# Kernel tuning notes

Hardware: AMD Instinct MI355X
Metric: run time of the kernel (lower is better)

## Reference

```python
import jax, jax.numpy as jnp
import numpy as np

IN_FEATURES = 1024
OUT_FEATURES = 1024
NUM_GRIDS = 8
GRID_MIN, GRID_MAX = -2.0, 2.0
DENOM = (GRID_MAX - GRID_MIN) / (NUM_GRIDS - 1)
LN_EPS = 1e-5
GRID = jnp.linspace(GRID_MIN, GRID_MAX, NUM_GRIDS)


def setup_inputs() -> dict:
    key = jax.random.key(0)
    k_x, k_sw, k_bw = jax.random.split(key, 3)
    N = 8192
    x = jax.random.normal(k_x, (N, IN_FEATURES), dtype=jnp.float32)
    ln_gamma = jnp.ones((IN_FEATURES,), dtype=jnp.float32)
    ln_beta = jnp.zeros((IN_FEATURES,), dtype=jnp.float32)
    # trunc_normal(std=0.1) approximated by scaled normal
    spline_w = 0.1 * jax.random.normal(k_sw, (OUT_FEATURES, IN_FEATURES * NUM_GRIDS), dtype=jnp.float32)
    base_w = jax.random.normal(k_bw, (OUT_FEATURES, IN_FEATURES), dtype=jnp.float32) * (1.0 / np.sqrt(IN_FEATURES))
    base_b = jnp.zeros((OUT_FEATURES,), dtype=jnp.float32)
    return {"x": x, "ln_gamma": ln_gamma, "ln_beta": ln_beta,
            "spline_w": spline_w, "base_w": base_w, "base_b": base_b}


def reference(x, ln_gamma, ln_beta, spline_w, base_w, base_b):
    # LayerNorm over last dim
    mu = jnp.mean(x, axis=-1, keepdims=True)
    var = jnp.var(x, axis=-1, keepdims=True)
    xn = (x - mu) * jax.lax.rsqrt(var + LN_EPS) * ln_gamma + ln_beta
    # RBF basis: [N, in, G]
    basis = jnp.exp(-jnp.square((xn[..., None] - GRID) / DENOM))
    basis = basis.reshape(x.shape[0], IN_FEATURES * NUM_GRIDS)
    y = jnp.einsum('nk,ok->no', basis, spline_w)
    y = y + jnp.einsum('nd,od->no', jax.nn.silu(x), base_w) + base_b
    return y
```

## Files before the change

kernel.cpp:

```cpp
#include <hip/hip_runtime.h>
#include <hip/hip_bf16.h>
#include <stdint.h>

#define IN_F 1024
#define OUT_F 1024
#define NG 8
#define KSPLINE 8192
#define KDIM 9216
#define KHALF 4608
#define M_ROWS 8192
#define LOG2E 1.4426950408889634f
#define KC 2.1019642153762872f

#define A_BLOCKS (M_ROWS / 4)
#define W_BLOCKS ((OUT_F * 2304) / 256)
#define RB (KDIM * 2)
#define GBOFF 131072

using half4v = __attribute__((ext_vector_type(4))) _Float16;
using half8  = __attribute__((ext_vector_type(8))) _Float16;
using f32x4  = __attribute__((ext_vector_type(4))) float;
using f32x2  = __attribute__((ext_vector_type(2))) float;

#define AS1 __attribute__((address_space(1)))
#define AS3 __attribute__((address_space(3)))

__global__ __launch_bounds__(256) void prep_kernel(
        const float* __restrict__ x, const float* __restrict__ sw,
        const float* __restrict__ bw, _Float16* __restrict__ S,
        float* __restrict__ musig, _Float16* __restrict__ W) {
    if (blockIdx.x >= A_BLOCKS) {
        int idx = (blockIdx.x - A_BLOCKS) * 256 + threadIdx.x;
        int o   = idx / 2304;
        int k4  = idx - o * 2304;
        f32x4 v;
        if (k4 < 2048) v = __builtin_nontemporal_load(&((const f32x4*)sw)[(size_t)o * 2048 + k4]);
        else           v = __builtin_nontemporal_load(&((const f32x4*)bw)[(size_t)o * 256 + (k4 - 2048)]);
        half4v h = { (_Float16)v.x, (_Float16)v.y, (_Float16)v.z, (_Float16)v.w };
        *(half4v*)(W + (size_t)idx * 4) = h;
        return;
    }
    const int wave = threadIdx.x >> 6, lane = threadIdx.x & 63;
    const int row = blockIdx.x * 4 + wave;
    const float* xr = x + (size_t)row * IN_F;

    float xv[16];
    float s = 0.0f, s2 = 0.0f;
#pragma unroll
    for (int j = 0; j < 16; ++j) {
        float v = xr[j * 64 + lane];
        xv[j] = v;
        s += v;
        s2 += v * v;
    }
#pragma unroll
    for (int off = 32; off > 0; off >>= 1) {
        s  += __shfl_xor(s, off);
        s2 += __shfl_xor(s2, off);
    }
    float mu   = s * (1.0f / IN_F);
    float var  = s2 * (1.0f / IN_F) - mu * mu;
    float rstd = rsqrtf(var + 1e-5f);
    if (lane == 0) {
        f32x2 ms; ms[0] = mu; ms[1] = rstd;
        ((f32x2*)musig)[row] = ms;
    }
    _Float16* Srow = S + (size_t)row * IN_F;
#pragma unroll
    for (int j = 0; j < 16; ++j) {
        float xs = xv[j];
        Srow[j * 64 + lane] = (_Float16)(xs / (1.0f + exp2f(-xs * LOG2E)));
    }
}

__device__ __forceinline__ half8 spline8(float xv, float mu, float rs, float gk, float bk) {
    const float cqg[8] = {
        -2.0000000f * KC, -1.4285715f * KC, -0.8571429f * KC, -0.2857143f * KC,
         0.2857143f * KC,  0.8571429f * KC,  1.4285715f * KC,  2.0000000f * KC };
    float xq = fmaf((xv - mu) * rs, gk, bk);
    half8 h;
#pragma unroll
    for (int g = 0; g < 8; ++g) {
        float d = xq - cqg[g];
        h[g] = (_Float16)__builtin_amdgcn_exp2f(-(d * d));
    }
    return h;
}

__global__ __launch_bounds__(512, 2) void gemm_kernel(
        const _Float16* __restrict__ W, const _Float16* __restrict__ S,
        const float* __restrict__ x, const float* __restrict__ musig,
        const float* __restrict__ gamma, const float* __restrict__ beta,
        const float* __restrict__ bias, float* __restrict__ C,
        float* __restrict__ P, int ntiles, int gpz) {
    extern __shared__ __align__(16) char smem[];
    const int tid  = threadIdx.x;
    const int wave = tid >> 6, lane = tid & 63;
    const int wm = wave >> 2, wn = wave & 3;

    const int lb = blockIdx.x;
    const int per_xcd = gridDim.x >> 5;
    const int xcd = lb & 7, sl = lb >> 3;
    const int g  = xcd * per_xcd + (sl >> 2);
    const int bn = sl & 3;
    const int bm = g / gpz;
    const int z  = g - bm * gpz;
    const int ksoff = z * KHALF;

    const int l8 = lane >> 3;
    const int chunkswz = ((lane & 7) ^ l8) << 4;
    const int gAr[4] = {0, 128, 64, 192};
    const int gB[4]  = {0, 128, 32, 160};
    const char* pB[4];
    const char* pS[4];
    const float* xp[4];
#pragma unroll
    for (int s = 0; s < 4; ++s) {
        pB[s] = (const char*)W + (size_t)(bn * 256 + gB[s] + (wave >> 2) * 64
                + (wave & 3) * 8 + l8) * RB + (size_t)ksoff * 2 + chunkswz;
        int arow = bm * 256 + gAr[s] + wave * 8 + l8;
        pS[s] = (const char*)S + (size_t)arow * (IN_F * 2) + chunkswz;
    }
    const int r6 = tid >> 3;
    const int c8 = tid & 7;
    const int wAbase = r6 * 128 + ((c8 ^ (r6 & 7)) << 4);
    float mu4[4], rs4[4];
#pragma unroll
    for (int s = 0; s < 4; ++s) {
        int arow = bm * 256 + gAr[s] + r6;
        xp[s] = x + (size_t)arow * IN_F;
        f32x2 ms = ((const f32x2*)musig)[arow];
        mu4[s] = ms[0]; rs4[s] = ms[1];
    }

#define STAGE_B(s, nb, colb) __builtin_amdgcn_global_load_lds( \
        (const AS1 void*)(pB[s] + (colb)), \
        (AS3 void*)(smem + (nb) + 32768 + (s) * 8192 + wave * 1024), 16, 0, 0)
#define STAGE_S(s, nb, colb) __builtin_amdgcn_global_load_lds( \
        (const AS1 void*)(pS[s] + (colb)), \
        (AS3 void*)(smem + (nb) + (s) * 8192 + wave * 1024), 16, 0, 0)

    const int lm  = lane & 15;
    const int hi  = (lane >> 4) << 4;
    const int swz = (lm & 7) << 4;
    const int ck0 = (0  + hi) ^ swz;
    const int ck1 = (64 + hi) ^ swz;
    const int aB0 = (0 + wm) * 8192 + lm * 128;
    const int aB1 = (2 + wm) * 8192 + lm * 128;
    const int bB0 = 32768 + (0 + (wn >> 1)) * 8192 + ((wn & 1) * 32 + lm) * 128;
    const int bB1 = 32768 + (2 + (wn >> 1)) * 8192 + ((wn & 1) * 32 + lm) * 128;

    f32x4 acc[8][4] = {};

#define MFMA_QUAD(MB, NB2, Aa, Bb)                                              \
    __builtin_amdgcn_s_barrier();                                               \
    asm volatile("s_waitcnt lgkmcnt(0)" ::: "memory");                          \
    __builtin_amdgcn_sched_barrier(0);                                          \
    __builtin_amdgcn_s_setprio(1);                                              \
    _Pragma("unroll")                                                           \
    for (int n = 0; n < 2; ++n)                                                 \
        _Pragma("unroll")                                                       \
        for (int m = 0; m < 4; ++m)                                             \
            acc[(MB)+m][(NB2)+n] = __builtin_amdgcn_mfma_f32_16x16x32_f16(      \
                Aa[m][0], Bb[n][0], acc[(MB)+m][(NB2)+n], 0, 0, 0);             \
    _Pragma("unroll")                                                           \
    for (int n = 0; n < 2; ++n)                                                 \
        _Pragma("unroll")                                                       \
        for (int m = 0; m < 4; ++m)                                             \
            acc[(MB)+m][(NB2)+n] = __builtin_amdgcn_mfma_f32_16x16x32_f16(      \
                Aa[m][1], Bb[n][1], acc[(MB)+m][(NB2)+n], 0, 0, 0);             \
    __builtin_amdgcn_s_setprio(0);                                              \
    __builtin_amdgcn_s_barrier();

    {
        f32x2 t0; t0[0] = gamma[tid] * KC;       t0[1] = beta[tid] * KC;
        f32x2 t1; t1[0] = gamma[tid + 512] * KC; t1[1] = beta[tid + 512] * KC;
        *(f32x2*)(smem + GBOFF + tid * 8) = t0;
        *(f32x2*)(smem + GBOFF + (tid + 512) * 8) = t1;
    }
    const int f00 = z * 576 + c8;
    float xf0[4];
#pragma unroll
    for (int s = 0; s < 4; ++s) xf0[s] = xp[s][f00];
    STAGE_B(0, 0, 0); STAGE_B(1, 0, 0); STAGE_B(2, 0, 0); STAGE_B(3, 0, 0);
    __syncthreads();
    {
        f32x2 gb0 = *(const f32x2*)(smem + GBOFF + f00 * 8);
#pragma unroll
        for (int s = 0; s < 4; ++s) {
            half8 h = spline8(xf0[s], mu4[s], rs4[s], gb0[0], gb0[1]);
            *(half8*)(smem + s * 8192 + wAbase) = h;
        }
    }
    asm volatile("s_waitcnt lgkmcnt(0)" ::: "memory");
    __builtin_amdgcn_s_barrier();

    for (int kt = 0; kt < ntiles; ++kt) {
        const int cb = (kt & 1) * 65536;
        const int nb = cb ^ 65536;
        const bool pref = (kt + 1 < ntiles);
        const int nk = ksoff + (kt + 1) * 64;
        const bool nsil = nk >= KSPLINE;
        const size_t bcolb = (size_t)(kt + 1) * 128;
        const int fb = z * 576 + (kt + 1) * 8 + c8;
        size_t scolb = 0;
        if (nsil) scolb = (size_t)(nk - KSPLINE) * 2;

        float xf[4];
        if (pref) {
            if (nsil) { STAGE_S(0, nb, scolb); STAGE_S(1, nb, scolb); }
            else {
#pragma unroll
                for (int s = 0; s < 4; ++s) xf[s] = xp[s][fb];
            }
        }
        half8 aF[4][2], bF[2][2];
#pragma unroll
        for (int m = 0; m < 4; ++m) {
            aF[m][0] = *(const half8*)(smem + cb + aB0 + m * 2048 + ck0);
            aF[m][1] = *(const half8*)(smem + cb + aB0 + m * 2048 + ck1);
        }
#pragma unroll
        for (int n = 0; n < 2; ++n) {
            bF[n][0] = *(const half8*)(smem + cb + bB0 + n * 2048 + ck0);
            bF[n][1] = *(const half8*)(smem + cb + bB0 + n * 2048 + ck1);
        }
        if (pref) {
            if (nsil) asm volatile("s_waitcnt vmcnt(2)" ::: "memory");
            else      asm volatile("s_waitcnt vmcnt(4)" ::: "memory");
        } else {
            asm volatile("s_waitcnt vmcnt(0)" ::: "memory");
        }
        asm volatile("s_waitcnt lgkmcnt(8)" ::: "memory");
        MFMA_QUAD(0, 0, aF, bF)

        half8 bG[2][2];
#pragma unroll
        for (int n = 0; n < 2; ++n) {
            bG[n][0] = *(const half8*)(smem + cb + bB1 + n * 2048 + ck0);
            bG[n][1] = *(const half8*)(smem + cb + bB1 + n * 2048 + ck1);
        }
        if (pref) { STAGE_B(0, nb, bcolb); STAGE_B(1, nb, bcolb); }
        MFMA_QUAD(0, 2, aF, bG)

        half8 aG[4][2];
#pragma unroll
        for (int m = 0; m < 4; ++m) {
            aG[m][0] = *(const half8*)(smem + cb + aB1 + m * 2048 + ck0);
            aG[m][1] = *(const half8*)(smem + cb + aB1 + m * 2048 + ck1);
        }
        f32x2 gb;
        if (pref) {
            if (!nsil) {
                gb = *(const f32x2*)(smem + GBOFF + fb * 8);
                half8 h0 = spline8(xf[0], mu4[0], rs4[0], gb[0], gb[1]);
                half8 h1 = spline8(xf[1], mu4[1], rs4[1], gb[0], gb[1]);
                *(half8*)(smem + nb + 0 * 8192 + wAbase) = h0;
                *(half8*)(smem + nb + 1 * 8192 + wAbase) = h1;
            }
            STAGE_B(2, nb, bcolb); STAGE_B(3, nb, bcolb);
        }
        MFMA_QUAD(4, 0, aG, bF)

        if (pref) {
            if (!nsil) {
                half8 h2 = spline8(xf[2], mu4[2], rs4[2], gb[0], gb[1]);
                half8 h3 = spline8(xf[3], mu4[3], rs4[3], gb[0], gb[1]);
                *(half8*)(smem + nb + 2 * 8192 + wAbase) = h2;
                *(half8*)(smem + nb + 3 * 8192 + wAbase) = h3;
            }
            asm volatile("s_waitcnt vmcnt(2)" ::: "memory");
            if (nsil) { STAGE_S(2, nb, scolb); STAGE_S(3, nb, scolb); }
        } else {
            asm volatile("s_waitcnt vmcnt(0)" ::: "memory");
        }
        asm volatile("s_waitcnt lgkmcnt(0)" ::: "memory");
        MFMA_QUAD(4, 2, aG, bG)
    }

    const int cn  = lane & 15;
    const int rm4 = (lane >> 4) * 4;
    float* dst = z ? P : C;
#pragma unroll
    for (int nf = 0; nf < 4; ++nf) {
        int col = bn * 256 + wn * 64 + nf * 16 + cn;
        float bv = z ? 0.0f : bias[col];
#pragma unroll
        for (int mf = 0; mf < 8; ++mf) {
            int row = bm * 256 + wm * 128 + mf * 16 + rm4;
            float* cp = dst + (size_t)row * OUT_F + col;
#pragma unroll
            for (int r = 0; r < 4; ++r)
                cp[(size_t)r * OUT_F] = acc[mf][nf][r] + bv;
        }
    }
}

__global__ __launch_bounds__(256) void reduce_kernel(float* __restrict__ C,
        const float* __restrict__ P) {
    const int n4 = M_ROWS * OUT_F / 4;
    float4* c4 = (float4*)C;
    const float4* p4 = (const float4*)P;
    for (int i = blockIdx.x * 256 + threadIdx.x; i < n4; i += 2048 * 256) {
        float4 a = c4[i];
        float4 b = p4[i];
        a.x += b.x; a.y += b.y; a.z += b.z; a.w += b.w;
        c4[i] = a;
    }
}

extern "C" void kernel_launch(void* const* d_in, const int* in_sizes, int n_in,
                              void* d_out, int out_size, void* d_ws, size_t ws_size,
                              hipStream_t stream) {
    const float* x     = (const float*)d_in[0];
    const float* gamma = (const float*)d_in[1];
    const float* beta  = (const float*)d_in[2];
    const float* sw    = (const float*)d_in[3];
    const float* bw    = (const float*)d_in[4];
    const float* bb    = (const float*)d_in[5];
    float* out = (float*)d_out;

    char* ws = (char*)d_ws;
    size_t offW = 0;
    size_t offS = (size_t)OUT_F * KDIM * 2;
    size_t offM = offS + (size_t)M_ROWS * IN_F * 2;
    size_t offP = offM + (size_t)M_ROWS * 8;
    size_t need = offP + (size_t)M_ROWS * OUT_F * 4;
    _Float16* Wb = (_Float16*)(ws + offW);
    _Float16* Sb = (_Float16*)(ws + offS);
    float*    Mb = (float*)(ws + offM);
    float*    Pb = (float*)(ws + offP);
    const int split = (ws_size >= need);

    static int s_attr = 0;
    if (!s_attr) {
        (void)hipFuncSetAttribute(reinterpret_cast<const void*>(gemm_kernel),
                            hipFuncAttributeMaxDynamicSharedMemorySize, 139264);
        s_attr = 1;
    }

    prep_kernel<<<A_BLOCKS + W_BLOCKS, 256, 0, stream>>>(
        x, sw, bw, Sb, Mb, Wb);
    if (split) {
        gemm_kernel<<<256, 512, 139264, stream>>>(
            Wb, Sb, x, Mb, gamma, beta, bb, out, Pb, KHALF / 64, 2);
        reduce_kernel<<<2048, 256, 0, stream>>>(out, Pb);
    } else {
        gemm_kernel<<<128, 512, 139264, stream>>>(
            Wb, Sb, x, Mb, gamma, beta, bb, out, Pb, KDIM / 64, 1);
    }
}
```

Before: 315.3 us.

## Interleave RBF basis computation inside MFMA blocks and use recurrence for Gaussians

The RBF basis generation for the next tile now runs between the two k-halves of the MFMA sequences, inside the prioritized region, rather than in separate gaps between quads. The intent is to hide the VALU and transcendental work behind matrix-core execution. The eight Gaussians per input are now produced with two exp2 calls plus a multiplicative recurrence (a geometric ratio chain) instead of eight exp2 calls, which cuts transcendental throughput pressure. The recurrence adds a small rounding error that accumulates across the chain, and the new ordering changes how LDS writes line up with the barriers.

```diff
diff --git a/kernel.cpp b/kernel.cpp
--- a/kernel.cpp
+++ b/kernel.cpp
@@ -11,6 +11,10 @@
 #define M_ROWS 8192
 #define LOG2E 1.4426950408889634f
 #define KC 2.1019642153762872f
+#define CQ0 (-2.0f * KC)
+#define DQ  (0.5714285714285714f * KC)
+#define DQ2 1.4426950408889634f
+#define QCHAIN 0.1353352832366127f
 
 #define A_BLOCKS (M_ROWS / 4)
 #define W_BLOCKS ((OUT_F * 2304) / 256)
@@ -73,16 +77,15 @@
     }
 }
 
-__device__ __forceinline__ half8 spline8(float xv, float mu, float rs, float gk, float bk) {
-    const float cqg[8] = {
-        -2.0000000f * KC, -1.4285715f * KC, -0.8571429f * KC, -0.2857143f * KC,
-         0.2857143f * KC,  0.8571429f * KC,  1.4285715f * KC,  2.0000000f * KC };
-    float xq = fmaf((xv - mu) * rs, gk, bk);
+__device__ __forceinline__ half8 spline8c(float xq) {
+    float d0 = xq - CQ0;
+    float b  = __builtin_amdgcn_exp2f(-(d0 * d0));
+    float r  = __builtin_amdgcn_exp2f(fmaf(2.0f * DQ, d0, -DQ2));
     half8 h;
 #pragma unroll
     for (int g = 0; g < 8; ++g) {
-        float d = xq - cqg[g];
-        h[g] = (_Float16)__builtin_amdgcn_exp2f(-(d * d));
+        h[g] = (_Float16)b;
+        if (g < 7) { b = b * r; r = r * QCHAIN; }
     }
     return h;
 }
@@ -118,8 +121,8 @@
     for (int s = 0; s < 4; ++s) {
         pB[s] = (const char*)W + (size_t)(bn * 256 + gB[s] + (wave >> 2) * 64
                 + (wave & 3) * 8 + l8) * RB + (size_t)ksoff * 2 + chunkswz;
-        int arow = bm * 256 + gAr[s] + wave * 8 + l8;
-        pS[s] = (const char*)S + (size_t)arow * (IN_F * 2) + chunkswz;
+        pS[s] = (const char*)S + (size_t)(bm * 256 + gAr[s] + wave * 8 + l8)
+                * (IN_F * 2) + chunkswz;
     }
     const int r6 = tid >> 3;
     const int c8 = tid & 7;
@@ -152,23 +155,20 @@
 
     f32x4 acc[8][4] = {};
 
-#define MFMA_QUAD(MB, NB2, Aa, Bb)                                              \
-    __builtin_amdgcn_s_barrier();                                               \
-    asm volatile("s_waitcnt lgkmcnt(0)" ::: "memory");                          \
-    __builtin_amdgcn_sched_barrier(0);                                          \
-    __builtin_amdgcn_s_setprio(1);                                              \
+#define MFMA_HALF(MB, NB2, Aa, Bb, KH)                                          \
     _Pragma("unroll")                                                           \
     for (int n = 0; n < 2; ++n)                                                 \
         _Pragma("unroll")                                                       \
         for (int m = 0; m < 4; ++m)                                             \
             acc[(MB)+m][(NB2)+n] = __builtin_amdgcn_mfma_f32_16x16x32_f16(      \
-                Aa[m][0], Bb[n][0], acc[(MB)+m][(NB2)+n], 0, 0, 0);             \
-    _Pragma("unroll")                                                           \
-    for (int n = 0; n < 2; ++n)                                                 \
-        _Pragma("unroll")                                                       \
-        for (int m = 0; m < 4; ++m)                                             \
-            acc[(MB)+m][(NB2)+n] = __builtin_amdgcn_mfma_f32_16x16x32_f16(      \
-                Aa[m][1], Bb[n][1], acc[(MB)+m][(NB2)+n], 0, 0, 0);             \
+                Aa[m][KH], Bb[n][KH], acc[(MB)+m][(NB2)+n], 0, 0, 0);
+
+#define QUAD_OPEN()                                                             \
+    __builtin_amdgcn_s_barrier();                                               \
+    asm volatile("s_waitcnt lgkmcnt(0)" ::: "memory");                          \
+    __builtin_amdgcn_sched_barrier(0);                                          \
+    __builtin_amdgcn_s_setprio(1);
+#define QUAD_CLOSE()                                                            \
     __builtin_amdgcn_s_setprio(0);                                              \
     __builtin_amdgcn_s_barrier();
 
@@ -188,7 +188,7 @@
         f32x2 gb0 = *(const f32x2*)(smem + GBOFF + f00 * 8);
 #pragma unroll
         for (int s = 0; s < 4; ++s) {
-            half8 h = spline8(xf0[s], mu4[s], rs4[s], gb0[0], gb0[1]);
+            half8 h = spline8c(fmaf((xf0[s] - mu4[s]) * rs4[s], gb0[0], gb0[1]));
             *(half8*)(smem + s * 8192 + wAbase) = h;
         }
     }
@@ -232,7 +232,10 @@
             asm volatile("s_waitcnt vmcnt(0)" ::: "memory");
         }
         asm volatile("s_waitcnt lgkmcnt(8)" ::: "memory");
-        MFMA_QUAD(0, 0, aF, bF)
+        QUAD_OPEN();
+        MFMA_HALF(0, 0, aF, bF, 0)
+        MFMA_HALF(0, 0, aF, bF, 1)
+        QUAD_CLOSE();
 
         half8 bG[2][2];
 #pragma unroll
@@ -240,8 +243,13 @@
             bG[n][0] = *(const half8*)(smem + cb + bB1 + n * 2048 + ck0);
             bG[n][1] = *(const half8*)(smem + cb + bB1 + n * 2048 + ck1);
         }
+        f32x2 gb;
+        if (pref && !nsil) gb = *(const f32x2*)(smem + GBOFF + fb * 8);
         if (pref) { STAGE_B(0, nb, bcolb); STAGE_B(1, nb, bcolb); }
-        MFMA_QUAD(0, 2, aF, bG)
+        QUAD_OPEN();
+        MFMA_HALF(0, 2, aF, bG, 0)
+        MFMA_HALF(0, 2, aF, bG, 1)
+        QUAD_CLOSE();
 
         half8 aG[4][2];
 #pragma unroll
@@ -249,33 +257,34 @@
             aG[m][0] = *(const half8*)(smem + cb + aB1 + m * 2048 + ck0);
             aG[m][1] = *(const half8*)(smem + cb + aB1 + m * 2048 + ck1);
         }
-        f32x2 gb;
+        if (pref) { STAGE_B(2, nb, bcolb); STAGE_B(3, nb, bcolb); }
+        QUAD_OPEN();
+        MFMA_HALF(4, 0, aG, bF, 0)
+        if (pref && !nsil) {
+            half8 h0 = spline8c(fmaf((xf[0] - mu4[0]) * rs4[0], gb[0], gb[1]));
+            half8 h1 = spline8c(fmaf((xf[1] - mu4[1]) * rs4[1], gb[0], gb[1]));
+            *(half8*)(smem + nb + 0 * 8192 + wAbase) = h0;
+            *(half8*)(smem + nb + 1 * 8192 + wAbase) = h1;
+        }
+        MFMA_HALF(4, 0, aG, bF, 1)
+        QUAD_CLOSE();
+
         if (pref) {
-            if (!nsil) {
-                gb = *(const f32x2*)(smem + GBOFF + fb * 8);
-                half8 h0 = spline8(xf[0], mu4[0], rs4[0], gb[0], gb[1]);
-                half8 h1 = spline8(xf[1], mu4[1], rs4[1], gb[0], gb[1]);
-                *(half8*)(smem + nb + 0 * 8192 + wAbase) = h0;
-                *(half8*)(smem + nb + 1 * 8192 + wAbase) = h1;
-            }
-            STAGE_B(2, nb, bcolb); STAGE_B(3, nb, bcolb);
-        }
-        MFMA_QUAD(4, 0, aG, bF)
-
-        if (pref) {
-            if (!nsil) {
-                half8 h2 = spline8(xf[2], mu4[2], rs4[2], gb[0], gb[1]);
-                half8 h3 = spline8(xf[3], mu4[3], rs4[3], gb[0], gb[1]);
-                *(half8*)(smem + nb + 2 * 8192 + wAbase) = h2;
-                *(half8*)(smem + nb + 3 * 8192 + wAbase) = h3;
-            }
             asm volatile("s_waitcnt vmcnt(2)" ::: "memory");
             if (nsil) { STAGE_S(2, nb, scolb); STAGE_S(3, nb, scolb); }
         } else {
             asm volatile("s_waitcnt vmcnt(0)" ::: "memory");
         }
-        asm volatile("s_waitcnt lgkmcnt(0)" ::: "memory");
-        MFMA_QUAD(4, 2, aG, bG)
+        QUAD_OPEN();
+        MFMA_HALF(4, 2, aG, bG, 0)
+        if (pref && !nsil) {
+            half8 h2 = spline8c(fmaf((xf[2] - mu4[2]) * rs4[2], gb[0], gb[1]));
+            half8 h3 = spline8c(fmaf((xf[3] - mu4[3]) * rs4[3], gb[0], gb[1]));
+            *(half8*)(smem + nb + 2 * 8192 + wAbase) = h2;
+            *(half8*)(smem + nb + 3 * 8192 + wAbase) = h3;
+        }
+        MFMA_HALF(4, 2, aG, bG, 1)
+        QUAD_CLOSE();
     }
 
     const int cn  = lane & 15;
```

New measurement: 304.2 us. -3.5%, faster.
